# Performance work log

Hardware: AMD Instinct MI355X
Metric: run time of the kernel (lower is better)

The kernel has to match this reference:

```python
import jax, jax.numpy as jnp
import numpy as np

B, N, C = 8, 1024, 768
NUM_HEADS = 12
HEAD_DIM = C // NUM_HEADS  # 64
WS = 32                    # window_size[0] == window_size[1] == H == W
REL_DIM = 2 * WS - 1       # 63


def setup_inputs() -> dict:
    key = jax.random.key(0)
    ks = jax.random.split(key, 7)
    x = jax.random.normal(ks[0], (B, N, C), dtype=jnp.float32)
    qkv_w = jax.random.normal(ks[1], (3 * C, C), dtype=jnp.float32) * 0.02
    qkv_b = jnp.zeros((3 * C,), dtype=jnp.float32)
    proj_w = jax.random.normal(ks[2], (C, C), dtype=jnp.float32) * 0.02
    proj_b = jnp.zeros((C,), dtype=jnp.float32)
    rel_pos_h = jax.random.normal(ks[3], (REL_DIM, HEAD_DIM), dtype=jnp.float32) * 0.02
    rel_pos_w = jax.random.normal(ks[4], (REL_DIM, HEAD_DIM), dtype=jnp.float32) * 0.02
    return {
        "x": x,
        "qkv_w": qkv_w,
        "qkv_b": qkv_b,
        "proj_w": proj_w,
        "proj_b": proj_b,
        "rel_pos_h": rel_pos_h,
        "rel_pos_w": rel_pos_w,
        "H": WS,
        "W": WS,
    }


def reference(x, qkv_w, qkv_b, proj_w, proj_b, rel_pos_h, rel_pos_w, H, W):
    B_, N_, C_ = x.shape
    heads = NUM_HEADS
    hd = C_ // heads
    scale = hd ** -0.5

    # qkv projection: (B, N, 3, heads, hd) -> (3, B, heads, N, hd)
    qkv = (x @ qkv_w.T + qkv_b).reshape(B_, N_, 3, heads, hd).transpose(2, 0, 3, 1, 4)
    q, k, v = qkv[0], qkv[1], qkv[2]
    q = q * scale

    # raw scores (B, heads, N, N)
    attn = jnp.einsum('bhqd,bhkd->bhqk', q, k)

    # decomposed relative position bias (q_shape == k_shape -> ratios are 1.0)
    dist_h = jnp.arange(H)[:, None] - jnp.arange(H)[None, :] + (H - 1)
    dist_w = jnp.arange(W)[:, None] - jnp.arange(W)[None, :] + (W - 1)
    Rh = rel_pos_h[dist_h]  # (H, H, hd)
    Rw = rel_pos_w[dist_w]  # (W, W, hd)

    r_q = q.reshape(B_, heads, H, W, hd)
    rel_h = jnp.einsum('byhwc,hkc->byhwk', r_q, Rh)  # (B, heads, H, W, k_h)
    rel_w = jnp.einsum('byhwc,wkc->byhwk', r_q, Rw)  # (B, heads, H, W, k_w)

    attn = (attn.reshape(B_, heads, H, W, H, W)
            + rel_h[:, :, :, :, :, None]
            + rel_w[:, :, :, :, None, :]).reshape(B_, heads, N_, N_)

    attn = jax.nn.softmax(attn, axis=-1)
    out = jnp.einsum('bhqk,bhkd->bhqd', attn, v)
    out = out.transpose(0, 2, 1, 3).reshape(B_, N_, heads * hd)
    return out @ proj_w.T + proj_b
```

## Files before the change

kernel.cpp:

```cpp
#include <hip/hip_runtime.h>
#include <cstddef>

typedef short s4v __attribute__((ext_vector_type(4)));
typedef short s8v __attribute__((ext_vector_type(8)));
typedef float f4v __attribute__((ext_vector_type(4)));

__device__ __forceinline__ unsigned short f2bf(float f) {
    union { float f; unsigned u; } v; v.f = f;
    unsigned r = v.u + 0x7fff + ((v.u >> 16) & 1);
    return (unsigned short)(r >> 16);
}
__device__ __forceinline__ float bf2f(unsigned short u) {
    union { unsigned u; float f; } v; v.u = ((unsigned)u) << 16;
    return v.f;
}

__device__ __forceinline__ void gl_lds16(const void* g, void* l) {
    __builtin_amdgcn_global_load_lds(
        (const __attribute__((address_space(1))) void*)g,
        (__attribute__((address_space(3))) void*)l, 16, 0, 0);
}

#define QSC   0.18033688011112043f
#define EOFF  23.082320654223414f

__global__ __launch_bounds__(256) void to_bf16_all(
    const float* __restrict__ x, const float* __restrict__ qw,
    const float* __restrict__ pw, unsigned short* __restrict__ xd,
    unsigned short* __restrict__ qd, unsigned short* __restrict__ pd)
{
    int i = blockIdx.x * 256 + threadIdx.x;
    const float* s; unsigned short* d; int j;
    if (i < 786432)       { s = x;  d = xd; j = i; }
    else if (i < 1007616) { s = qw; d = qd; j = i - 786432; }
    else                  { s = pw; d = pd; j = i - 1007616; }
    float4 f0 = ((const float4*)s)[j * 2];
    float4 f1 = ((const float4*)s)[j * 2 + 1];
    uint4 pk;
    pk.x = (unsigned)f2bf(f0.x) | ((unsigned)f2bf(f0.y) << 16);
    pk.y = (unsigned)f2bf(f0.z) | ((unsigned)f2bf(f0.w) << 16);
    pk.z = (unsigned)f2bf(f1.x) | ((unsigned)f2bf(f1.y) << 16);
    pk.w = (unsigned)f2bf(f1.z) | ((unsigned)f2bf(f1.w) << 16);
    ((uint4*)d)[j] = pk;
}

__global__ __launch_bounds__(256) void qkv_gemm_mfma(
    const unsigned short* __restrict__ A, const unsigned short* __restrict__ W,
    const float* __restrict__ bias,
    unsigned short* __restrict__ qb, unsigned short* __restrict__ kb,
    unsigned short* __restrict__ vt)
{
    __shared__ __align__(16) unsigned short As[128 * 32];
    __shared__ __align__(16) unsigned short Bs[128 * 32];
    const int t     = threadIdx.x;
    const int bc    = blockIdx.x;
    const int br    = blockIdx.y;
    const int wv    = t >> 6;
    const int lane  = t & 63;
    const int col16 = lane & 15;
    const int quad  = lane >> 4;
    const int w4    = lane >> 2;
    const int k8    = (lane & 3) << 3;
    const int mw    = wv >> 1, nw = wv & 1;

    const unsigned short* Ag = A + (size_t)(br * 128 + (wv << 5) + w4) * 768 + k8;
    const unsigned short* Wg = W + (size_t)(bc * 128 + (wv << 5) + w4) * 768 + k8;
    unsigned short* Asw = &As[(wv << 5) * 32];
    unsigned short* Bsw = &Bs[(wv << 5) * 32];

    f4v acc[4][4];
#pragma unroll
    for (int mt = 0; mt < 4; ++mt)
#pragma unroll
        for (int nt = 0; nt < 4; ++nt) {
            acc[mt][nt][0] = 0.f; acc[mt][nt][1] = 0.f;
            acc[mt][nt][2] = 0.f; acc[mt][nt][3] = 0.f;
        }

    for (int k0 = 0; k0 < 768; k0 += 32) {
        __syncthreads();
        gl_lds16(Ag + k0,             Asw);
        gl_lds16(Ag + k0 + 16 * 768,  Asw + 16 * 32);
        gl_lds16(Wg + k0,             Bsw);
        gl_lds16(Wg + k0 + 16 * 768,  Bsw + 16 * 32);
        __syncthreads();

        s8v a[4], b[4];
#pragma unroll
        for (int mt = 0; mt < 4; ++mt)
            a[mt] = *(const s8v*)&As[(mw * 64 + mt * 16 + col16) * 32 + quad * 8];
#pragma unroll
        for (int nt = 0; nt < 4; ++nt)
            b[nt] = *(const s8v*)&Bs[(nw * 64 + nt * 16 + col16) * 32 + quad * 8];
#pragma unroll
        for (int mt = 0; mt < 4; ++mt)
#pragma unroll
            for (int nt = 0; nt < 4; ++nt)
                acc[mt][nt] = __builtin_amdgcn_mfma_f32_16x16x32_bf16(
                    a[mt], b[nt], acc[mt][nt], 0, 0, 0);
    }

    const int which = bc / 6;
    const int cb    = (bc % 6) * 128 + nw * 64;
    const int m0    = br * 128 + mw * 64 + quad * 4;
    if (which == 2) {
#pragma unroll
        for (int nt = 0; nt < 4; ++nt) {
            int c    = cb + nt * 16 + col16;
            int head = c >> 6, d = c & 63;
            float bv = bias[1536 + c];
#pragma unroll
            for (int mt = 0; mt < 4; ++mt) {
                int mb  = m0 + mt * 16;
                int bbk = mb >> 10, tok = mb & 1023;
                uint2 pk;
                pk.x = (unsigned)f2bf(acc[mt][nt][0] + bv)
                     | ((unsigned)f2bf(acc[mt][nt][1] + bv) << 16);
                pk.y = (unsigned)f2bf(acc[mt][nt][2] + bv)
                     | ((unsigned)f2bf(acc[mt][nt][3] + bv) << 16);
                *(uint2*)&vt[((size_t)(bbk * 12 + head)) * 65536 + (size_t)d * 1024 + tok] = pk;
            }
        }
    } else {
        const float sc = (which == 0) ? QSC : 1.0f;
        unsigned short* dst = (which == 0) ? qb : kb;
#pragma unroll
        for (int nt = 0; nt < 4; ++nt) {
            int c    = cb + nt * 16 + col16;
            int head = c >> 6, d = c & 63;
            float bv = bias[which * 768 + c];
#pragma unroll
            for (int mt = 0; mt < 4; ++mt) {
#pragma unroll
                for (int i = 0; i < 4; ++i) {
                    int m   = m0 + mt * 16 + i;
                    int bbk = m >> 10, tok = m & 1023;
                    dst[(((size_t)(bbk * 12 + head) << 10) + tok) * 64 + d] =
                        f2bf((acc[mt][nt][i] + bv) * sc);
                }
            }
        }
    }
}

__global__ __launch_bounds__(256) void proj_gemm_mfma(
    const unsigned short* __restrict__ A, const unsigned short* __restrict__ W,
    const float* __restrict__ bias, float* __restrict__ Out)
{
    __shared__ __align__(16) unsigned short As[128 * 32];
    __shared__ __align__(16) unsigned short Bs[128 * 32];
    const int t     = threadIdx.x;
    const int bc    = blockIdx.x;
    const int br    = blockIdx.y;
    const int wv    = t >> 6;
    const int lane  = t & 63;
    const int col16 = lane & 15;
    const int quad  = lane >> 4;
    const int w4    = lane >> 2;
    const int k8    = (lane & 3) << 3;
    const int mw    = wv >> 1, nw = wv & 1;

    const unsigned short* Ag = A + (size_t)(br * 128 + (wv << 5) + w4) * 768 + k8;
    const unsigned short* Wg = W + (size_t)(bc * 128 + (wv << 5) + w4) * 768 + k8;
    unsigned short* Asw = &As[(wv << 5) * 32];
    unsigned short* Bsw = &Bs[(wv << 5) * 32];

    f4v acc[4][4];
#pragma unroll
    for (int mt = 0; mt < 4; ++mt)
#pragma unroll
        for (int nt = 0; nt < 4; ++nt) {
            acc[mt][nt][0] = 0.f; acc[mt][nt][1] = 0.f;
            acc[mt][nt][2] = 0.f; acc[mt][nt][3] = 0.f;
        }

    for (int k0 = 0; k0 < 768; k0 += 32) {
        __syncthreads();
        gl_lds16(Ag + k0,             Asw);
        gl_lds16(Ag + k0 + 16 * 768,  Asw + 16 * 32);
        gl_lds16(Wg + k0,             Bsw);
        gl_lds16(Wg + k0 + 16 * 768,  Bsw + 16 * 32);
        __syncthreads();

        s8v a[4], b[4];
#pragma unroll
        for (int mt = 0; mt < 4; ++mt)
            a[mt] = *(const s8v*)&As[(mw * 64 + mt * 16 + col16) * 32 + quad * 8];
#pragma unroll
        for (int nt = 0; nt < 4; ++nt)
            b[nt] = *(const s8v*)&Bs[(nw * 64 + nt * 16 + col16) * 32 + quad * 8];
#pragma unroll
        for (int mt = 0; mt < 4; ++mt)
#pragma unroll
            for (int nt = 0; nt < 4; ++nt)
                acc[mt][nt] = __builtin_amdgcn_mfma_f32_16x16x32_bf16(
                    a[mt], b[nt], acc[mt][nt], 0, 0, 0);
    }

    const int m0 = br * 128 + mw * 64 + quad * 4;
#pragma unroll
    for (int nt = 0; nt < 4; ++nt) {
        int c    = bc * 128 + nw * 64 + nt * 16 + col16;
        float bv = bias[c];
#pragma unroll
        for (int mt = 0; mt < 4; ++mt) {
#pragma unroll
            for (int i = 0; i < 4; ++i) {
                int m = m0 + mt * 16 + i;
                Out[(size_t)m * 768 + c] = acc[mt][nt][i] + bv;
            }
        }
    }
}

__global__ __launch_bounds__(256) void bias_prep_mfma(
    const unsigned short* __restrict__ Q, const float* __restrict__ Rh,
    const float* __restrict__ Rw, unsigned short* __restrict__ qhb,
    unsigned short* __restrict__ qwb)
{
    __shared__ __align__(16) char smem[36864];
    unsigned short (*Qs)[72]  = (unsigned short (*)[72])smem;
    unsigned short (*Rs)[72]  = (unsigned short (*)[72])(smem + 18432);
    unsigned short (*Wsm)[72] = (unsigned short (*)[72])(smem + 27648);
    float (*G)[66]            = (float (*)[66])smem;

    const int t    = threadIdx.x;
    const int tc8  = blockIdx.x;
    const int bh   = blockIdx.y;
    const int tok0 = tc8 << 7;

    for (int id = t; id < 1024; id += 256) {
        int row = id >> 3, g8 = (id & 7) << 3;
        *(uint4*)&Qs[row][g8] =
            *(const uint4*)(Q + ((size_t)bh * 1024 + tok0 + row) * 64 + g8);
    }
    for (int id = t; id < 512; id += 256) {
        int row = id >> 3, g8 = (id & 7) << 3;
        unsigned short* dh = &Rs[row][g8];
        unsigned short* dw = &Wsm[row][g8];
        if (row < 63) {
            const float* sh = Rh + row * 64 + g8;
            const float* sw = Rw + row * 64 + g8;
            float4 a = *(const float4*)sh; float4 b = *(const float4*)(sh + 4);
            float4 c = *(const float4*)sw; float4 d = *(const float4*)(sw + 4);
            dh[0] = f2bf(a.x); dh[1] = f2bf(a.y); dh[2] = f2bf(a.z); dh[3] = f2bf(a.w);
            dh[4] = f2bf(b.x); dh[5] = f2bf(b.y); dh[6] = f2bf(b.z); dh[7] = f2bf(b.w);
            dw[0] = f2bf(c.x); dw[1] = f2bf(c.y); dw[2] = f2bf(c.z); dw[3] = f2bf(c.w);
            dw[4] = f2bf(d.x); dw[5] = f2bf(d.y); dw[6] = f2bf(d.z); dw[7] = f2bf(d.w);
        } else {
#pragma unroll
            for (int j = 0; j < 8; ++j) { dh[j] = 0; dw[j] = 0; }
        }
    }
    __syncthreads();

    const int wv    = t >> 6;
    const int lane  = t & 63;
    const int col16 = lane & 15;
    const int quad  = lane >> 4;
    const int r0    = wv << 5;

    s8v qa[2][2], rb[4][2], wb[4][2];
#pragma unroll
    for (int mt = 0; mt < 2; ++mt)
#pragma unroll
        for (int kc = 0; kc < 2; ++kc)
            qa[mt][kc] = *(const s8v*)&Qs[r0 + mt * 16 + col16][kc * 32 + quad * 8];
#pragma unroll
    for (int nt = 0; nt < 4; ++nt)
#pragma unroll
        for (int kc = 0; kc < 2; ++kc) {
            rb[nt][kc] = *(const s8v*)&Rs[nt * 16 + col16][kc * 32 + quad * 8];
            wb[nt][kc] = *(const s8v*)&Wsm[nt * 16 + col16][kc * 32 + quad * 8];
        }

    f4v ah[2][4], aw[2][4];
#pragma unroll
    for (int mt = 0; mt < 2; ++mt)
#pragma unroll
        for (int nt = 0; nt < 4; ++nt) {
            f4v z; z[0] = 0.f; z[1] = 0.f; z[2] = 0.f; z[3] = 0.f;
            ah[mt][nt] = z; aw[mt][nt] = z;
        }
#pragma unroll
    for (int mt = 0; mt < 2; ++mt)
#pragma unroll
        for (int nt = 0; nt < 4; ++nt) {
            ah[mt][nt] = __builtin_amdgcn_mfma_f32_16x16x32_bf16(qa[mt][0], rb[nt][0], ah[mt][nt], 0, 0, 0);
            ah[mt][nt] = __builtin_amdgcn_mfma_f32_16x16x32_bf16(qa[mt][1], rb[nt][1], ah[mt][nt], 0, 0, 0);
            aw[mt][nt] = __builtin_amdgcn_mfma_f32_16x16x32_bf16(qa[mt][0], wb[nt][0], aw[mt][nt], 0, 0, 0);
            aw[mt][nt] = __builtin_amdgcn_mfma_f32_16x16x32_bf16(qa[mt][1], wb[nt][1], aw[mt][nt], 0, 0, 0);
        }
    __syncthreads();

#pragma unroll
    for (int mt = 0; mt < 2; ++mt)
#pragma unroll
        for (int nt = 0; nt < 4; ++nt)
#pragma unroll
            for (int i = 0; i < 4; ++i)
                G[r0 + mt * 16 + quad * 4 + i][nt * 16 + col16] = ah[mt][nt][i];
    __syncthreads();
    for (int id = t; id < 2048; id += 256) {
        int tok = id >> 4, c2 = (id & 15) << 1;
        int i_img = (tc8 << 2) + (tok >> 5);
        float g0 = G[tok][i_img - c2 + 31];
        float g1 = G[tok][i_img - c2 + 30];
        unsigned pk = (unsigned)f2bf(g0) | ((unsigned)f2bf(g1) << 16);
        *(unsigned*)&qhb[(((size_t)bh << 10) + tok0 + tok) * 32 + c2] = pk;
    }
    __syncthreads();

#pragma unroll
    for (int mt = 0; mt < 2; ++mt)
#pragma unroll
        for (int nt = 0; nt < 4; ++nt)
#pragma unroll
            for (int i = 0; i < 4; ++i)
                G[r0 + mt * 16 + quad * 4 + i][nt * 16 + col16] = aw[mt][nt][i];
    __syncthreads();
    for (int id = t; id < 2048; id += 256) {
        int tok = id >> 4, c2 = (id & 15) << 1;
        int j = tok & 31;
        float g0 = G[tok][j - c2 + 31];
        float g1 = G[tok][j - c2 + 30];
        unsigned pk = (unsigned)f2bf(g0) | ((unsigned)f2bf(g1) << 16);
        *(unsigned*)&qwb[(((size_t)bh << 10) + tok0 + tok) * 32 + c2] = pk;
    }
}

__global__ __launch_bounds__(256, 4) void attn_mfma(
    const unsigned short* __restrict__ Q, const unsigned short* __restrict__ K,
    const unsigned short* __restrict__ Vt,
    const unsigned short* __restrict__ qhb, const unsigned short* __restrict__ qwb,
    unsigned short* __restrict__ Out)
{
    const int t  = threadIdx.x;
    const int id  = blockIdx.x;
    const int xcd = id & 7;
    const int wq  = id >> 3;
    const int bh  = xcd * 12 + (wq % 12);
    const int qt2 = wq / 12;
    const int b   = bh / 12;
    const int h   = bh - b * 12;
    const int q0  = qt2 << 6;

    __shared__ __align__(16) unsigned short Ks[64 * 72];
    __shared__ __align__(16) unsigned short Vs[64 * 72];
    __shared__ __align__(16) unsigned short Pl[64 * 68];
    __shared__ float qh_s[64][33];

    const unsigned short* Kp = K  + (size_t)bh * 65536;
    const unsigned short* Vp = Vt + (size_t)bh * 65536;

    {
        const unsigned* qhp = (const unsigned*)(qhb + ((size_t)bh * 1024 + q0) * 32);
        for (int i2 = t; i2 < 1024; i2 += 256) {
            int row = i2 >> 4, c2 = (i2 & 15) << 1;
            unsigned ph = qhp[i2];
            qh_s[row][c2]     = bf2f((unsigned short)(ph & 0xffff)) - EOFF;
            qh_s[row][c2 + 1] = bf2f((unsigned short)(ph >> 16))    - EOFF;
        }
    }

    const int wv    = t >> 6;
    const int lane  = t & 63;
    const int col16 = lane & 15;
    const int quad  = lane >> 4;
    const int qrow0 = wv << 4;

    s8v qa0, qa1;
    {
        const unsigned short* qsrc =
            Q + ((size_t)bh * 1024 + q0 + qrow0 + col16) * 64 + quad * 8;
        qa0 = *(const s8v*)qsrc;
        qa1 = *(const s8v*)(qsrc + 32);
    }

    float qwr[4][2];
#pragma unroll
    for (int i = 0; i < 4; ++i) {
        size_t row = (size_t)bh * 1024 + q0 + qrow0 + quad * 4 + i;
        qwr[i][0] = bf2f(qwb[row * 32 + col16]);
        qwr[i][1] = bf2f(qwb[row * 32 + col16 + 16]);
    }

    {
        uint4 pk0, pk1, pv0, pv1;
        int e0 = t * 8, e1 = t * 8 + 2048;
        pk0 = *(const uint4*)(Kp + e0);
        pk1 = *(const uint4*)(Kp + e1);
        pv0 = *(const uint4*)(Vp + (size_t)(e0 >> 6) * 1024 + (e0 & 63));
        pv1 = *(const uint4*)(Vp + (size_t)(e1 >> 6) * 1024 + (e1 & 63));
        *(uint4*)&Ks[(e0 >> 6) * 72 + (e0 & 63)] = pk0;
        *(uint4*)&Ks[(e1 >> 6) * 72 + (e1 & 63)] = pk1;
        *(uint4*)&Vs[(e0 >> 6) * 72 + (e0 & 63)] = pv0;
        *(uint4*)&Vs[(e1 >> 6) * 72 + (e1 & 63)] = pv1;
    }
    __syncthreads();

    f4v o[4];
#pragma unroll
    for (int nt = 0; nt < 4; ++nt) { o[nt][0] = 0.f; o[nt][1] = 0.f; o[nt][2] = 0.f; o[nt][3] = 0.f; }
    float lp[4] = {0.f, 0.f, 0.f, 0.f};

    const int e0 = t * 8, e1 = t * 8 + 2048;
    for (int kt = 0; kt < 16; ++kt) {
        uint4 pk0, pk1, pv0, pv1;
        if (kt < 15) {
            const int k0n = (kt + 1) << 6;
            pk0 = *(const uint4*)(Kp + (size_t)k0n * 64 + e0);
            pk1 = *(const uint4*)(Kp + (size_t)k0n * 64 + e1);
            pv0 = *(const uint4*)(Vp + (size_t)(e0 >> 6) * 1024 + k0n + (e0 & 63));
            pv1 = *(const uint4*)(Vp + (size_t)(e1 >> 6) * 1024 + k0n + (e1 & 63));
        }

        f4v s4a[4];
#pragma unroll
        for (int nt = 0; nt < 4; ++nt) {
            s8v b0 = *(const s8v*)&Ks[(nt * 16 + col16) * 72 + quad * 8];
            s8v b1 = *(const s8v*)&Ks[(nt * 16 + col16) * 72 + 32 + quad * 8];
            f4v acc; acc[0] = 0.f; acc[1] = 0.f; acc[2] = 0.f; acc[3] = 0.f;
            acc = __builtin_amdgcn_mfma_f32_16x16x32_bf16(qa0, b0, acc, 0, 0, 0);
            acc = __builtin_amdgcn_mfma_f32_16x16x32_bf16(qa1, b1, acc, 0, 0, 0);
            s4a[nt] = acc;
        }

        float qh0[4], qh1[4];
#pragma unroll
        for (int i = 0; i < 4; ++i) {
            qh0[i] = qh_s[qrow0 + quad * 4 + i][(kt << 1) + 0];
            qh1[i] = qh_s[qrow0 + quad * 4 + i][(kt << 1) + 1];
        }

#pragma unroll
        for (int nt = 0; nt < 4; ++nt) {
#pragma unroll
            for (int i = 0; i < 4; ++i) {
                float s  = s4a[nt][i] + ((nt < 2) ? qh0[i] : qh1[i]) + qwr[i][nt & 1];
                float pe = __builtin_amdgcn_exp2f(s);
                lp[i] += pe;
                Pl[(qrow0 + quad * 4 + i) * 68 + nt * 16 + col16] = f2bf(pe);
            }
        }
        asm volatile("s_waitcnt lgkmcnt(0)" ::: "memory");

        const unsigned short* prow = &Pl[(qrow0 + col16) * 68];
        s4v p0l = *(const s4v*)(prow + quad * 8);
        s4v p0h = *(const s4v*)(prow + quad * 8 + 4);
        s4v p1l = *(const s4v*)(prow + 32 + quad * 8);
        s4v p1h = *(const s4v*)(prow + 36 + quad * 8);
        s8v pa0 = __builtin_shufflevector(p0l, p0h, 0, 1, 2, 3, 4, 5, 6, 7);
        s8v pa1 = __builtin_shufflevector(p1l, p1h, 0, 1, 2, 3, 4, 5, 6, 7);
#pragma unroll
        for (int nt = 0; nt < 4; ++nt) {
            s8v vb0 = *(const s8v*)&Vs[(nt * 16 + col16) * 72 + quad * 8];
            s8v vb1 = *(const s8v*)&Vs[(nt * 16 + col16) * 72 + 32 + quad * 8];
            o[nt] = __builtin_amdgcn_mfma_f32_16x16x32_bf16(pa0, vb0, o[nt], 0, 0, 0);
            o[nt] = __builtin_amdgcn_mfma_f32_16x16x32_bf16(pa1, vb1, o[nt], 0, 0, 0);
        }

        __syncthreads();
        if (kt < 15) {
            *(uint4*)&Ks[(e0 >> 6) * 72 + (e0 & 63)] = pk0;
            *(uint4*)&Ks[(e1 >> 6) * 72 + (e1 & 63)] = pk1;
            *(uint4*)&Vs[(e0 >> 6) * 72 + (e0 & 63)] = pv0;
            *(uint4*)&Vs[(e1 >> 6) * 72 + (e1 & 63)] = pv1;
        }
        __syncthreads();
    }

#pragma unroll
    for (int i = 0; i < 4; ++i) {
#pragma unroll
        for (int m = 8; m >= 1; m >>= 1) lp[i] += __shfl_xor(lp[i], m, 16);
    }
#pragma unroll
    for (int i = 0; i < 4; ++i) {
        float inv = 1.f / lp[i];
        int   qr  = q0 + qrow0 + quad * 4 + i;
        unsigned short* dst = Out + ((size_t)b * 1024 + qr) * 768 + h * 64;
#pragma unroll
        for (int nt = 0; nt < 4; ++nt)
            dst[nt * 16 + col16] = f2bf(o[nt][i] * inv);
    }
}

extern "C" void kernel_launch(void* const* d_in, const int* in_sizes, int n_in,
                              void* d_out, int out_size, void* d_ws, size_t ws_size,
                              hipStream_t stream) {
    const float* x      = (const float*)d_in[0];
    const float* qkv_w  = (const float*)d_in[1];
    const float* qkv_b  = (const float*)d_in[2];
    const float* proj_w = (const float*)d_in[3];
    const float* proj_b = (const float*)d_in[4];
    const float* rel_h  = (const float*)d_in[5];
    const float* rel_w  = (const float*)d_in[6];
    float* out = (float*)d_out;

    char* ws = (char*)d_ws;
    unsigned short* qbuf  = (unsigned short*)(ws);
    unsigned short* kbuf  = (unsigned short*)(ws + 12582912);
    unsigned short* vtbuf = (unsigned short*)(ws + 25165824);
    unsigned short* xab   = (unsigned short*)(ws + 37748736);
    unsigned short* wqb   = (unsigned short*)(ws + 50331648);
    unsigned short* wpb   = (unsigned short*)(ws + 53870592);
    unsigned short* qhb   = (unsigned short*)(ws + 55050240);
    unsigned short* qwb   = (unsigned short*)(ws + 61341696);

    to_bf16_all<<<4224, 256, 0, stream>>>(x, qkv_w, proj_w, xab, wqb, wpb);
    qkv_gemm_mfma<<<dim3(18, 64), 256, 0, stream>>>(xab, wqb, qkv_b, qbuf, kbuf, vtbuf);
    bias_prep_mfma<<<dim3(8, 96), 256, 0, stream>>>(qbuf, rel_h, rel_w, qhb, qwb);
    attn_mfma<<<1536, 256, 0, stream>>>(qbuf, kbuf, vtbuf, qhb, qwb, xab);
    proj_gemm_mfma<<<dim3(6, 64), 256, 0, stream>>>(xab, wpb, proj_b, out);
}
```

Baseline: 240.3 us.

## Split attention keys across waves and compute S transposed to skip LDS staging

The attention kernel now gives each block 32 queries, so the grid doubles, and splits the key range across the four waves instead of splitting queries. Each wave computes K·Q^T so that the MFMA output layout feeds straight into the P·V MFMA operand, using a permuted key order. This drops the LDS P buffer and the K/V shared-memory staging with its two barriers per step; K and V fragments are loaded directly from global memory. The cost is a cross-wave reduction of the partial outputs and row sums through LDS at the end, more global traffic per block since K/V are no longer shared across waves, and more registers (launch bound lowered to 3).

```diff
diff --git a/kernel.cpp b/kernel.cpp
--- a/kernel.cpp
+++ b/kernel.cpp
@@ -329,160 +329,150 @@
     }
 }
 
-__global__ __launch_bounds__(256, 4) void attn_mfma(
+__global__ __launch_bounds__(256, 3) void attn_mfma(
     const unsigned short* __restrict__ Q, const unsigned short* __restrict__ K,
     const unsigned short* __restrict__ Vt,
     const unsigned short* __restrict__ qhb, const unsigned short* __restrict__ qwb,
     unsigned short* __restrict__ Out)
 {
-    const int t  = threadIdx.x;
+    const int t   = threadIdx.x;
     const int id  = blockIdx.x;
     const int xcd = id & 7;
     const int wq  = id >> 3;
     const int bh  = xcd * 12 + (wq % 12);
-    const int qt2 = wq / 12;
+    const int qt  = wq / 12;
     const int b   = bh / 12;
     const int h   = bh - b * 12;
-    const int q0  = qt2 << 6;
-
-    __shared__ __align__(16) unsigned short Ks[64 * 72];
-    __shared__ __align__(16) unsigned short Vs[64 * 72];
-    __shared__ __align__(16) unsigned short Pl[64 * 68];
-    __shared__ float qh_s[64][33];
+    const int q0  = qt << 5;
+
+    __shared__ __align__(16) float qh_s[32][33];
+    __shared__ __align__(16) float Obuf[4][32][68];
+    __shared__ float red[4][32];
 
     const unsigned short* Kp = K  + (size_t)bh * 65536;
     const unsigned short* Vp = Vt + (size_t)bh * 65536;
 
     {
-        const unsigned* qhp = (const unsigned*)(qhb + ((size_t)bh * 1024 + q0) * 32);
-        for (int i2 = t; i2 < 1024; i2 += 256) {
-            int row = i2 >> 4, c2 = (i2 & 15) << 1;
-            unsigned ph = qhp[i2];
-            qh_s[row][c2]     = bf2f((unsigned short)(ph & 0xffff)) - EOFF;
-            qh_s[row][c2 + 1] = bf2f((unsigned short)(ph >> 16))    - EOFF;
-        }
-    }
-
-    const int wv    = t >> 6;
-    const int lane  = t & 63;
-    const int col16 = lane & 15;
-    const int quad  = lane >> 4;
-    const int qrow0 = wv << 4;
-
-    s8v qa0, qa1;
+        int row = t >> 3, c4 = (t & 7) << 2;
+        const unsigned short* src = qhb + ((size_t)bh * 1024 + q0 + row) * 32 + c4;
+        uint2 pk = *(const uint2*)src;
+        qh_s[row][c4 + 0] = bf2f((unsigned short)(pk.x & 0xffff)) - EOFF;
+        qh_s[row][c4 + 1] = bf2f((unsigned short)(pk.x >> 16))    - EOFF;
+        qh_s[row][c4 + 2] = bf2f((unsigned short)(pk.y & 0xffff)) - EOFF;
+        qh_s[row][c4 + 3] = bf2f((unsigned short)(pk.y >> 16))    - EOFF;
+    }
+
+    const int wv = t >> 6, lane = t & 63, c = lane & 15, qd = lane >> 4;
+
+    s8v qf[2][2];
+    float uw[2][8];
+#pragma unroll
+    for (int mt = 0; mt < 2; ++mt) {
+        const unsigned short* qp =
+            Q + ((size_t)bh * 1024 + q0 + mt * 16 + c) * 64 + qd * 8;
+        qf[mt][0] = *(const s8v*)qp;
+        qf[mt][1] = *(const s8v*)(qp + 32);
+        const unsigned short* wp =
+            qwb + ((size_t)bh * 1024 + q0 + mt * 16 + c) * 32 + qd * 8;
+        s8v w8 = *(const s8v*)wp;
+#pragma unroll
+        for (int j = 0; j < 8; ++j) uw[mt][j] = bf2f((unsigned short)w8[j]);
+    }
+    __syncthreads();
+
+    const int perm0 = ((c >> 2) << 3) | (c & 3);
+
+    f4v o[2][4];
+#pragma unroll
+    for (int mt = 0; mt < 2; ++mt)
+#pragma unroll
+        for (int dt = 0; dt < 4; ++dt) {
+            o[mt][dt][0] = 0.f; o[mt][dt][1] = 0.f;
+            o[mt][dt][2] = 0.f; o[mt][dt][3] = 0.f;
+        }
+    float lp[2] = {0.f, 0.f};
+
+#pragma unroll 2
+    for (int kt = 0; kt < 8; ++kt) {
+        const int bt = (kt << 7) + (wv << 5);
+        const unsigned short* k0p = Kp + (size_t)(bt + perm0) * 64 + qd * 8;
+        s8v ka0  = *(const s8v*)k0p;
+        s8v ka0b = *(const s8v*)(k0p + 32);
+        s8v ka1  = *(const s8v*)(k0p + 256);
+        s8v ka1b = *(const s8v*)(k0p + 288);
+        s8v vb[4];
+#pragma unroll
+        for (int dt = 0; dt < 4; ++dt)
+            vb[dt] = *(const s8v*)(Vp + (size_t)(dt * 16 + c) * 1024 + bt + qd * 8);
+
+        float qhv0 = qh_s[c][(kt << 2) + wv];
+        float qhv1 = qh_s[16 + c][(kt << 2) + wv];
+
+        s8v pa[2];
+#pragma unroll
+        for (int mt = 0; mt < 2; ++mt) {
+            const float qhv = mt ? qhv1 : qhv0;
+            f4v c0, c1;
+            c0[0] = 0.f; c0[1] = 0.f; c0[2] = 0.f; c0[3] = 0.f;
+            c1[0] = 0.f; c1[1] = 0.f; c1[2] = 0.f; c1[3] = 0.f;
+            c0 = __builtin_amdgcn_mfma_f32_16x16x32_bf16(ka0,  qf[mt][0], c0, 0, 0, 0);
+            c0 = __builtin_amdgcn_mfma_f32_16x16x32_bf16(ka0b, qf[mt][1], c0, 0, 0, 0);
+            c1 = __builtin_amdgcn_mfma_f32_16x16x32_bf16(ka1,  qf[mt][0], c1, 0, 0, 0);
+            c1 = __builtin_amdgcn_mfma_f32_16x16x32_bf16(ka1b, qf[mt][1], c1, 0, 0, 0);
+            s8v p;
+#pragma unroll
+            for (int j = 0; j < 4; ++j) {
+                float pe = __builtin_amdgcn_exp2f(c0[j] + qhv + uw[mt][j]);
+                lp[mt] += pe;
+                p[j] = (short)f2bf(pe);
+            }
+#pragma unroll
+            for (int j = 0; j < 4; ++j) {
+                float pe = __builtin_amdgcn_exp2f(c1[j] + qhv + uw[mt][4 + j]);
+                lp[mt] += pe;
+                p[4 + j] = (short)f2bf(pe);
+            }
+            pa[mt] = p;
+        }
+#pragma unroll
+        for (int mt = 0; mt < 2; ++mt)
+#pragma unroll
+            for (int dt = 0; dt < 4; ++dt)
+                o[mt][dt] = __builtin_amdgcn_mfma_f32_16x16x32_bf16(
+                    pa[mt], vb[dt], o[mt][dt], 0, 0, 0);
+    }
+
+#pragma unroll
+    for (int mt = 0; mt < 2; ++mt) {
+        lp[mt] += __shfl_xor(lp[mt], 16);
+        lp[mt] += __shfl_xor(lp[mt], 32);
+    }
+    if (qd == 0) { red[wv][c] = lp[0]; red[wv][16 + c] = lp[1]; }
+#pragma unroll
+    for (int mt = 0; mt < 2; ++mt)
+#pragma unroll
+        for (int dt = 0; dt < 4; ++dt)
+#pragma unroll
+            for (int r = 0; r < 4; ++r)
+                Obuf[wv][mt * 16 + qd * 4 + r][dt * 16 + c] = o[mt][dt][r];
+    __syncthreads();
+
     {
-        const unsigned short* qsrc =
-            Q + ((size_t)bh * 1024 + q0 + qrow0 + col16) * 64 + quad * 8;
-        qa0 = *(const s8v*)qsrc;
-        qa1 = *(const s8v*)(qsrc + 32);
-    }
-
-    float qwr[4][2];
-#pragma unroll
-    for (int i = 0; i < 4; ++i) {
-        size_t row = (size_t)bh * 1024 + q0 + qrow0 + quad * 4 + i;
-        qwr[i][0] = bf2f(qwb[row * 32 + col16]);
-        qwr[i][1] = bf2f(qwb[row * 32 + col16 + 16]);
-    }
-
-    {
-        uint4 pk0, pk1, pv0, pv1;
-        int e0 = t * 8, e1 = t * 8 + 2048;
-        pk0 = *(const uint4*)(Kp + e0);
-        pk1 = *(const uint4*)(Kp + e1);
-        pv0 = *(const uint4*)(Vp + (size_t)(e0 >> 6) * 1024 + (e0 & 63));
-        pv1 = *(const uint4*)(Vp + (size_t)(e1 >> 6) * 1024 + (e1 & 63));
-        *(uint4*)&Ks[(e0 >> 6) * 72 + (e0 & 63)] = pk0;
-        *(uint4*)&Ks[(e1 >> 6) * 72 + (e1 & 63)] = pk1;
-        *(uint4*)&Vs[(e0 >> 6) * 72 + (e0 & 63)] = pv0;
-        *(uint4*)&Vs[(e1 >> 6) * 72 + (e1 & 63)] = pv1;
-    }
-    __syncthreads();
-
-    f4v o[4];
-#pragma unroll
-    for (int nt = 0; nt < 4; ++nt) { o[nt][0] = 0.f; o[nt][1] = 0.f; o[nt][2] = 0.f; o[nt][3] = 0.f; }
-    float lp[4] = {0.f, 0.f, 0.f, 0.f};
-
-    const int e0 = t * 8, e1 = t * 8 + 2048;
-    for (int kt = 0; kt < 16; ++kt) {
-        uint4 pk0, pk1, pv0, pv1;
-        if (kt < 15) {
-            const int k0n = (kt + 1) << 6;
-            pk0 = *(const uint4*)(Kp + (size_t)k0n * 64 + e0);
-            pk1 = *(const uint4*)(Kp + (size_t)k0n * 64 + e1);
-            pv0 = *(const uint4*)(Vp + (size_t)(e0 >> 6) * 1024 + k0n + (e0 & 63));
-            pv1 = *(const uint4*)(Vp + (size_t)(e1 >> 6) * 1024 + k0n + (e1 & 63));
-        }
-
-        f4v s4a[4];
-#pragma unroll
-        for (int nt = 0; nt < 4; ++nt) {
-            s8v b0 = *(const s8v*)&Ks[(nt * 16 + col16) * 72 + quad * 8];
-            s8v b1 = *(const s8v*)&Ks[(nt * 16 + col16) * 72 + 32 + quad * 8];
-            f4v acc; acc[0] = 0.f; acc[1] = 0.f; acc[2] = 0.f; acc[3] = 0.f;
-            acc = __builtin_amdgcn_mfma_f32_16x16x32_bf16(qa0, b0, acc, 0, 0, 0);
-            acc = __builtin_amdgcn_mfma_f32_16x16x32_bf16(qa1, b1, acc, 0, 0, 0);
-            s4a[nt] = acc;
-        }
-
-        float qh0[4], qh1[4];
-#pragma unroll
-        for (int i = 0; i < 4; ++i) {
-            qh0[i] = qh_s[qrow0 + quad * 4 + i][(kt << 1) + 0];
-            qh1[i] = qh_s[qrow0 + quad * 4 + i][(kt << 1) + 1];
-        }
-
-#pragma unroll
-        for (int nt = 0; nt < 4; ++nt) {
-#pragma unroll
-            for (int i = 0; i < 4; ++i) {
-                float s  = s4a[nt][i] + ((nt < 2) ? qh0[i] : qh1[i]) + qwr[i][nt & 1];
-                float pe = __builtin_amdgcn_exp2f(s);
-                lp[i] += pe;
-                Pl[(qrow0 + quad * 4 + i) * 68 + nt * 16 + col16] = f2bf(pe);
-            }
-        }
-        asm volatile("s_waitcnt lgkmcnt(0)" ::: "memory");
-
-        const unsigned short* prow = &Pl[(qrow0 + col16) * 68];
-        s4v p0l = *(const s4v*)(prow + quad * 8);
-        s4v p0h = *(const s4v*)(prow + quad * 8 + 4);
-        s4v p1l = *(const s4v*)(prow + 32 + quad * 8);
-        s4v p1h = *(const s4v*)(prow + 36 + quad * 8);
-        s8v pa0 = __builtin_shufflevector(p0l, p0h, 0, 1, 2, 3, 4, 5, 6, 7);
-        s8v pa1 = __builtin_shufflevector(p1l, p1h, 0, 1, 2, 3, 4, 5, 6, 7);
-#pragma unroll
-        for (int nt = 0; nt < 4; ++nt) {
-            s8v vb0 = *(const s8v*)&Vs[(nt * 16 + col16) * 72 + quad * 8];
-            s8v vb1 = *(const s8v*)&Vs[(nt * 16 + col16) * 72 + 32 + quad * 8];
-            o[nt] = __builtin_amdgcn_mfma_f32_16x16x32_bf16(pa0, vb0, o[nt], 0, 0, 0);
-            o[nt] = __builtin_amdgcn_mfma_f32_16x16x32_bf16(pa1, vb1, o[nt], 0, 0, 0);
-        }
-
-        __syncthreads();
-        if (kt < 15) {
-            *(uint4*)&Ks[(e0 >> 6) * 72 + (e0 & 63)] = pk0;
-            *(uint4*)&Ks[(e1 >> 6) * 72 + (e1 & 63)] = pk1;
-            *(uint4*)&Vs[(e0 >> 6) * 72 + (e0 & 63)] = pv0;
-            *(uint4*)&Vs[(e1 >> 6) * 72 + (e1 & 63)] = pv1;
-        }
-        __syncthreads();
-    }
-
-#pragma unroll
-    for (int i = 0; i < 4; ++i) {
-#pragma unroll
-        for (int m = 8; m >= 1; m >>= 1) lp[i] += __shfl_xor(lp[i], m, 16);
-    }
-#pragma unroll
-    for (int i = 0; i < 4; ++i) {
-        float inv = 1.f / lp[i];
-        int   qr  = q0 + qrow0 + quad * 4 + i;
-        unsigned short* dst = Out + ((size_t)b * 1024 + qr) * 768 + h * 64;
-#pragma unroll
-        for (int nt = 0; nt < 4; ++nt)
-            dst[nt * 16 + col16] = f2bf(o[nt][i] * inv);
+        const int q = t >> 3, d8 = (t & 7) << 3;
+        float inv = 1.f / (red[0][q] + red[1][q] + red[2][q] + red[3][q]);
+        f4v s0 = *(const f4v*)&Obuf[0][q][d8];
+        f4v s1 = *(const f4v*)&Obuf[0][q][d8 + 4];
+#pragma unroll
+        for (int w = 1; w < 4; ++w) {
+            s0 += *(const f4v*)&Obuf[w][q][d8];
+            s1 += *(const f4v*)&Obuf[w][q][d8 + 4];
+        }
+        uint4 pk;
+        pk.x = (unsigned)f2bf(s0[0] * inv) | ((unsigned)f2bf(s0[1] * inv) << 16);
+        pk.y = (unsigned)f2bf(s0[2] * inv) | ((unsigned)f2bf(s0[3] * inv) << 16);
+        pk.z = (unsigned)f2bf(s1[0] * inv) | ((unsigned)f2bf(s1[1] * inv) << 16);
+        pk.w = (unsigned)f2bf(s1[2] * inv) | ((unsigned)f2bf(s1[3] * inv) << 16);
+        *(uint4*)(Out + ((size_t)b * 1024 + q0 + q) * 768 + h * 64 + d8) = pk;
     }
 }
 
@@ -511,6 +501,6 @@
     to_bf16_all<<<4224, 256, 0, stream>>>(x, qkv_w, proj_w, xab, wqb, wpb);
     qkv_gemm_mfma<<<dim3(18, 64), 256, 0, stream>>>(xab, wqb, qkv_b, qbuf, kbuf, vtbuf);
     bias_prep_mfma<<<dim3(8, 96), 256, 0, stream>>>(qbuf, rel_h, rel_w, qhb, qwb);
-    attn_mfma<<<1536, 256, 0, stream>>>(qbuf, kbuf, vtbuf, qhb, qwb, xab);
+    attn_mfma<<<3072, 256, 0, stream>>>(qbuf, kbuf, vtbuf, qhb, qwb, xab);
     proj_gemm_mfma<<<dim3(6, 64), 256, 0, stream>>>(xab, wpb, proj_b, out);
 }
```

Result: slower. 276.4 us (+15.0%).

## Compute transposed scores so P stays in registers, dropping LDS round-trip

Applied to the files above, without the earlier changes.

The QK^T MFMA now takes K as the A operand and Q as B, so each lane's score accumulator lines up with the A-operand layout the PV MFMA needs. The exponentiated probabilities are packed straight into bf16 MFMA operands in registers instead of being written to a shared P buffer and read back. K rows are stored in LDS under a permuted row order to make this key ordering work. The w-direction bias is loaded as one vector per lane, and the row-sum reduction becomes cross-quad shuffles plus a broadcast. This removes the P LDS traffic and its wait, but correctness depends on the K permutation matching the PV operand layout.

```diff
diff --git a/kernel.cpp b/kernel.cpp
--- a/kernel.cpp
+++ b/kernel.cpp
@@ -347,7 +347,6 @@
 
     __shared__ __align__(16) unsigned short Ks[64 * 72];
     __shared__ __align__(16) unsigned short Vs[64 * 72];
-    __shared__ __align__(16) unsigned short Pl[64 * 68];
     __shared__ float qh_s[64][33];
 
     const unsigned short* Kp = K  + (size_t)bh * 65536;
@@ -363,126 +362,119 @@
         }
     }
 
-    const int wv    = t >> 6;
-    const int lane  = t & 63;
-    const int col16 = lane & 15;
-    const int quad  = lane >> 4;
-    const int qrow0 = wv << 4;
-
-    s8v qa0, qa1;
+    const int wv = t >> 6;
+    const int lane = t & 63;
+    const int c  = lane & 15;
+    const int qd = lane >> 4;
+
+    s8v qf0, qf1;
+    float uw[8];
     {
-        const unsigned short* qsrc =
-            Q + ((size_t)bh * 1024 + q0 + qrow0 + col16) * 64 + quad * 8;
-        qa0 = *(const s8v*)qsrc;
-        qa1 = *(const s8v*)(qsrc + 32);
-    }
-
-    float qwr[4][2];
-#pragma unroll
-    for (int i = 0; i < 4; ++i) {
-        size_t row = (size_t)bh * 1024 + q0 + qrow0 + quad * 4 + i;
-        qwr[i][0] = bf2f(qwb[row * 32 + col16]);
-        qwr[i][1] = bf2f(qwb[row * 32 + col16 + 16]);
-    }
-
+        const size_t row = (size_t)bh * 1024 + q0 + (wv << 4) + c;
+        const unsigned short* qp = Q + row * 64 + qd * 8;
+        qf0 = *(const s8v*)qp;
+        qf1 = *(const s8v*)(qp + 32);
+        s8v w8 = *(const s8v*)(qwb + row * 32 + qd * 8);
+#pragma unroll
+        for (int j = 0; j < 8; ++j) uw[j] = bf2f((unsigned short)w8[j]);
+    }
+
+    const int e0 = t * 8, e1 = t * 8 + 2048;
+    const int g0 = e0 >> 6, g1 = e1 >> 6, s0 = e0 & 63, s1 = e1 & 63;
+    const int L0 = (g0 & 32) | ((g0 & 4) << 2) | ((g0 & 24) >> 1) | (g0 & 3);
+    const int L1 = (g1 & 32) | ((g1 & 4) << 2) | ((g1 & 24) >> 1) | (g1 & 3);
     {
-        uint4 pk0, pk1, pv0, pv1;
-        int e0 = t * 8, e1 = t * 8 + 2048;
-        pk0 = *(const uint4*)(Kp + e0);
-        pk1 = *(const uint4*)(Kp + e1);
-        pv0 = *(const uint4*)(Vp + (size_t)(e0 >> 6) * 1024 + (e0 & 63));
-        pv1 = *(const uint4*)(Vp + (size_t)(e1 >> 6) * 1024 + (e1 & 63));
-        *(uint4*)&Ks[(e0 >> 6) * 72 + (e0 & 63)] = pk0;
-        *(uint4*)&Ks[(e1 >> 6) * 72 + (e1 & 63)] = pk1;
-        *(uint4*)&Vs[(e0 >> 6) * 72 + (e0 & 63)] = pv0;
-        *(uint4*)&Vs[(e1 >> 6) * 72 + (e1 & 63)] = pv1;
+        uint4 pk0 = *(const uint4*)(Kp + e0);
+        uint4 pk1 = *(const uint4*)(Kp + e1);
+        uint4 pv0 = *(const uint4*)(Vp + (size_t)g0 * 1024 + s0);
+        uint4 pv1 = *(const uint4*)(Vp + (size_t)g1 * 1024 + s1);
+        *(uint4*)&Ks[L0 * 72 + s0] = pk0;
+        *(uint4*)&Ks[L1 * 72 + s1] = pk1;
+        *(uint4*)&Vs[g0 * 72 + s0] = pv0;
+        *(uint4*)&Vs[g1 * 72 + s1] = pv1;
     }
     __syncthreads();
 
     f4v o[4];
 #pragma unroll
-    for (int nt = 0; nt < 4; ++nt) { o[nt][0] = 0.f; o[nt][1] = 0.f; o[nt][2] = 0.f; o[nt][3] = 0.f; }
-    float lp[4] = {0.f, 0.f, 0.f, 0.f};
-
-    const int e0 = t * 8, e1 = t * 8 + 2048;
+    for (int dt = 0; dt < 4; ++dt) { o[dt][0] = 0.f; o[dt][1] = 0.f; o[dt][2] = 0.f; o[dt][3] = 0.f; }
+    float lp = 0.f;
+
     for (int kt = 0; kt < 16; ++kt) {
         uint4 pk0, pk1, pv0, pv1;
         if (kt < 15) {
             const int k0n = (kt + 1) << 6;
             pk0 = *(const uint4*)(Kp + (size_t)k0n * 64 + e0);
             pk1 = *(const uint4*)(Kp + (size_t)k0n * 64 + e1);
-            pv0 = *(const uint4*)(Vp + (size_t)(e0 >> 6) * 1024 + k0n + (e0 & 63));
-            pv1 = *(const uint4*)(Vp + (size_t)(e1 >> 6) * 1024 + k0n + (e1 & 63));
-        }
-
-        f4v s4a[4];
-#pragma unroll
-        for (int nt = 0; nt < 4; ++nt) {
-            s8v b0 = *(const s8v*)&Ks[(nt * 16 + col16) * 72 + quad * 8];
-            s8v b1 = *(const s8v*)&Ks[(nt * 16 + col16) * 72 + 32 + quad * 8];
-            f4v acc; acc[0] = 0.f; acc[1] = 0.f; acc[2] = 0.f; acc[3] = 0.f;
-            acc = __builtin_amdgcn_mfma_f32_16x16x32_bf16(qa0, b0, acc, 0, 0, 0);
-            acc = __builtin_amdgcn_mfma_f32_16x16x32_bf16(qa1, b1, acc, 0, 0, 0);
-            s4a[nt] = acc;
-        }
-
-        float qh0[4], qh1[4];
-#pragma unroll
-        for (int i = 0; i < 4; ++i) {
-            qh0[i] = qh_s[qrow0 + quad * 4 + i][(kt << 1) + 0];
-            qh1[i] = qh_s[qrow0 + quad * 4 + i][(kt << 1) + 1];
-        }
-
-#pragma unroll
-        for (int nt = 0; nt < 4; ++nt) {
-#pragma unroll
-            for (int i = 0; i < 4; ++i) {
-                float s  = s4a[nt][i] + ((nt < 2) ? qh0[i] : qh1[i]) + qwr[i][nt & 1];
-                float pe = __builtin_amdgcn_exp2f(s);
-                lp[i] += pe;
-                Pl[(qrow0 + quad * 4 + i) * 68 + nt * 16 + col16] = f2bf(pe);
-            }
-        }
-        asm volatile("s_waitcnt lgkmcnt(0)" ::: "memory");
-
-        const unsigned short* prow = &Pl[(qrow0 + col16) * 68];
-        s4v p0l = *(const s4v*)(prow + quad * 8);
-        s4v p0h = *(const s4v*)(prow + quad * 8 + 4);
-        s4v p1l = *(const s4v*)(prow + 32 + quad * 8);
-        s4v p1h = *(const s4v*)(prow + 36 + quad * 8);
-        s8v pa0 = __builtin_shufflevector(p0l, p0h, 0, 1, 2, 3, 4, 5, 6, 7);
-        s8v pa1 = __builtin_shufflevector(p1l, p1h, 0, 1, 2, 3, 4, 5, 6, 7);
-#pragma unroll
-        for (int nt = 0; nt < 4; ++nt) {
-            s8v vb0 = *(const s8v*)&Vs[(nt * 16 + col16) * 72 + quad * 8];
-            s8v vb1 = *(const s8v*)&Vs[(nt * 16 + col16) * 72 + 32 + quad * 8];
-            o[nt] = __builtin_amdgcn_mfma_f32_16x16x32_bf16(pa0, vb0, o[nt], 0, 0, 0);
-            o[nt] = __builtin_amdgcn_mfma_f32_16x16x32_bf16(pa1, vb1, o[nt], 0, 0, 0);
+            pv0 = *(const uint4*)(Vp + (size_t)g0 * 1024 + k0n + s0);
+            pv1 = *(const uint4*)(Vp + (size_t)g1 * 1024 + k0n + s1);
+        }
+
+        f4v sc[4];
+#pragma unroll
+        for (int T = 0; T < 4; ++T) {
+            s8v lo = *(const s8v*)&Ks[(T * 16 + c) * 72 + qd * 8];
+            s8v hi = *(const s8v*)&Ks[(T * 16 + c) * 72 + 32 + qd * 8];
+            f4v z; z[0] = 0.f; z[1] = 0.f; z[2] = 0.f; z[3] = 0.f;
+            z = __builtin_amdgcn_mfma_f32_16x16x32_bf16(lo, qf0, z, 0, 0, 0);
+            z = __builtin_amdgcn_mfma_f32_16x16x32_bf16(hi, qf1, z, 0, 0, 0);
+            sc[T] = z;
+        }
+
+        const float qhv0 = qh_s[(wv << 4) + c][(kt << 1)];
+        const float qhv1 = qh_s[(wv << 4) + c][(kt << 1) + 1];
+
+        s8v pa0, pa1;
+#pragma unroll
+        for (int j = 0; j < 4; ++j) {
+            float pe = __builtin_amdgcn_exp2f(sc[0][j] + qhv0 + uw[j]);
+            lp += pe; pa0[j] = (short)f2bf(pe);
+        }
+#pragma unroll
+        for (int j = 0; j < 4; ++j) {
+            float pe = __builtin_amdgcn_exp2f(sc[1][j] + qhv0 + uw[4 + j]);
+            lp += pe; pa0[4 + j] = (short)f2bf(pe);
+        }
+#pragma unroll
+        for (int j = 0; j < 4; ++j) {
+            float pe = __builtin_amdgcn_exp2f(sc[2][j] + qhv1 + uw[j]);
+            lp += pe; pa1[j] = (short)f2bf(pe);
+        }
+#pragma unroll
+        for (int j = 0; j < 4; ++j) {
+            float pe = __builtin_amdgcn_exp2f(sc[3][j] + qhv1 + uw[4 + j]);
+            lp += pe; pa1[4 + j] = (short)f2bf(pe);
+        }
+
+#pragma unroll
+        for (int dt = 0; dt < 4; ++dt) {
+            s8v vlo = *(const s8v*)&Vs[(dt * 16 + c) * 72 + qd * 8];
+            s8v vhi = *(const s8v*)&Vs[(dt * 16 + c) * 72 + 32 + qd * 8];
+            o[dt] = __builtin_amdgcn_mfma_f32_16x16x32_bf16(pa0, vlo, o[dt], 0, 0, 0);
+            o[dt] = __builtin_amdgcn_mfma_f32_16x16x32_bf16(pa1, vhi, o[dt], 0, 0, 0);
         }
 
         __syncthreads();
         if (kt < 15) {
-            *(uint4*)&Ks[(e0 >> 6) * 72 + (e0 & 63)] = pk0;
-            *(uint4*)&Ks[(e1 >> 6) * 72 + (e1 & 63)] = pk1;
-            *(uint4*)&Vs[(e0 >> 6) * 72 + (e0 & 63)] = pv0;
-            *(uint4*)&Vs[(e1 >> 6) * 72 + (e1 & 63)] = pv1;
+            *(uint4*)&Ks[L0 * 72 + s0] = pk0;
+            *(uint4*)&Ks[L1 * 72 + s1] = pk1;
+            *(uint4*)&Vs[g0 * 72 + s0] = pv0;
+            *(uint4*)&Vs[g1 * 72 + s1] = pv1;
         }
         __syncthreads();
     }
 
+    lp += __shfl_xor(lp, 16);
+    lp += __shfl_xor(lp, 32);
+
 #pragma unroll
     for (int i = 0; i < 4; ++i) {
-#pragma unroll
-        for (int m = 8; m >= 1; m >>= 1) lp[i] += __shfl_xor(lp[i], m, 16);
-    }
-#pragma unroll
-    for (int i = 0; i < 4; ++i) {
-        float inv = 1.f / lp[i];
-        int   qr  = q0 + qrow0 + quad * 4 + i;
+        float inv = 1.f / __shfl(lp, (qd << 2) + i);
+        int qr = q0 + (wv << 4) + (qd << 2) + i;
         unsigned short* dst = Out + ((size_t)b * 1024 + qr) * 768 + h * 64;
 #pragma unroll
-        for (int nt = 0; nt < 4; ++nt)
-            dst[nt * 16 + col16] = f2bf(o[nt][i] * inv);
+        for (int dt = 0; dt < 4; ++dt)
+            dst[dt * 16 + c] = f2bf(o[dt][i] * inv);
     }
 }
 
```

After: 226.1 us. -5.9%, faster.
